# Kernel optimization log

Hardware: AMD Instinct MI355X
Metric: run time of the kernel (lower is better)

The kernel has to match this reference:

```python
import jax, jax.numpy as jnp
import numpy as np

B, L, H, N, CH = 8, 2048, 512, 64, 1


def setup_inputs() -> dict:
    key = jax.random.key(0)
    ks = jax.random.split(key, 7)
    # S4D-Lin style init: w = -0.5 + i*pi*n, with slight noise on the real part
    w_re = -(0.5 + 0.1 * jax.random.uniform(ks[0], (H, N), dtype=jnp.float32))
    w_im = jnp.broadcast_to(jnp.pi * jnp.arange(N, dtype=jnp.float32), (H, N)).copy()
    C_re = jax.random.normal(ks[1], (CH, H, N), dtype=jnp.float32)
    C_im = jax.random.normal(ks[2], (CH, H, N), dtype=jnp.float32)
    D = jax.random.normal(ks[3], (CH, H), dtype=jnp.float32)
    # log-uniform dt in [1e-3, 1e-1]
    log_dt = jax.random.uniform(ks[4], (H,), dtype=jnp.float32,
                                minval=jnp.log(1e-3), maxval=jnp.log(1e-1))
    dt = jnp.exp(log_dt)
    u = jax.random.normal(ks[5], (B, L, H), dtype=jnp.float32)
    return {"u": u, "w_re": w_re, "w_im": w_im, "C_re": C_re,
            "C_im": C_im, "D": D, "dt": dt}


def reference(u, w_re, w_im, C_re, C_im, D, dt):
    # u: [B, L, H] -> [B, H, L]
    uT = jnp.swapaxes(u, -1, -2)
    l = uT.shape[-1]
    h = dt.shape[-1]
    w = (w_re + 1j * w_im).astype(jnp.complex64)          # [t, n]
    v = h // w.shape[0]
    w = jnp.tile(w, (v, 1))                                # [h, n]
    C = (C_re + 1j * C_im).astype(jnp.complex64)           # [c, h, n]
    # --- kernel generation ---
    dtA = w * dt[:, None]                                  # [h, n]
    K = jnp.arange(l) * dtA[..., None]                     # [h, n, l]
    Cs = C * ((jnp.exp(dtA) - 1.0) / w)                    # [c, h, n]
    k = 2.0 * jnp.einsum('chn,hnl->chl', Cs, jnp.exp(K)).real  # [c, h, l]
    # --- FFT convolution ---
    k_f = jnp.fft.rfft(k, n=2 * l - 1)                     # [c, h, l]
    u_f = jnp.fft.rfft(uT, n=2 * l - 1)                    # [B, h, l]
    y_f = jnp.einsum('...hl,chl->...chl', u_f, k_f)        # [B, c, h, l]
    y = jnp.fft.irfft(y_f, n=2 * l)[..., :l]               # [B, c, h, l]
    # skip connection
    y = y + jnp.einsum('...hl,ch->...chl', uT, D)
    # '... c h l -> ... l c h'
    return jnp.moveaxis(y, (-3, -2, -1), (-2, -1, -3))
```

## Files before the change

kernel.cpp:

```cpp
#include <hip/hip_runtime.h>
#include <hip/hip_bf16.h>
#include <math.h>


namespace {
constexpr int cB = 8;
constexpr int cL = 2048;
constexpr int cH = 512;
constexpr int cN = 64;
constexpr int M1 = 4095;
constexpr int M2 = 4096;
constexpr int BH = cB * cH;
constexpr int MA = BH + cH;

constexpr size_t S0   = 2 * ((size_t)cH * cN * 6);
constexpr size_t S_B1 = S0;
constexpr size_t S_A  = S_B1 + (size_t)4096 * 2048;
constexpr size_t S_T2 = S_A  + (size_t)MA * 2048;
constexpr size_t S_U  = S_T2 + (size_t)2048 * 4096;
}

typedef __attribute__((ext_vector_type(8))) short short8;
typedef __attribute__((ext_vector_type(4))) float f32x4;

static __device__ inline short f2bf(float x) {
    __hip_bfloat16 h = __float2bfloat16(x);
    return *reinterpret_cast<short*>(&h);
}
static __device__ inline float bf2f(short s) {
    return __uint_as_float(((unsigned int)(unsigned short)s) << 16);
}
static __device__ __forceinline__ void load_lds16(const short* g, short* l) {
    __builtin_amdgcn_global_load_lds(
        (const __attribute__((address_space(1))) void*)g,
        (__attribute__((address_space(3))) void*)l, 16, 0, 0);
}
#define WAIT_LGKM0() do { asm volatile("s_waitcnt lgkmcnt(0)" ::: "memory"); \
                          __builtin_amdgcn_sched_barrier(0); } while (0)
#define WAIT_LGKM(n) do { asm volatile("s_waitcnt lgkmcnt(" #n ")" ::: "memory"); \
                          __builtin_amdgcn_sched_barrier(0); } while (0)
#define WAIT_VM(n)   do { asm volatile("s_waitcnt vmcnt(" #n ")" ::: "memory"); \
                          __builtin_amdgcn_sched_barrier(0); } while (0)
#define BAR() __builtin_amdgcn_s_barrier()

__global__ __launch_bounds__(256) void k_tabs(short* __restrict__ Wb)
{
    int tid = threadIdx.x;
    if (blockIdx.x < 2048) {
        int j  = blockIdx.x;
        int base = (j < 1024) ? 4 * j : (j == 1024 ? 2 : 4 * (2048 - j) + 2);
        int t0 = tid * 8;
        int p0 = (int)(((long)j * t0) % M1);
        float c, s, cs, ss;
        sincosf((6.283185307179586f / (float)M1) * (float)p0, &s, &c);
        sincosf((6.283185307179586f / (float)M1) * (float)j,  &ss, &cs);
        short8 vc, vs;
#pragma unroll
        for (int i = 0; i < 8; ++i) {
            vc[i] = f2bf(c); vs[i] = f2bf(s);
            float tr = c * cs - s * ss;
            s = c * ss + s * cs;
            c = tr;
        }
        *(short8*)&Wb[S_B1 + (size_t)base       * 2048 + t0] = vc;
        *(short8*)&Wb[S_B1 + (size_t)(base + 1) * 2048 + t0] = vs;
    } else {
        int r   = blockIdx.x - 2048;
        int p   = r >> 10, tau = r & 1023;
        int t   = 2 * tau + p;
        int k0  = tid * 8;
        float stepang = (6.283185307179586f / (float)M2) * (float)t;
        float cs, ss; sincosf(stepang, &ss, &cs);
        short8 v;
        if (k0 < 1024) {
            int ph = (k0 * t) & (M2 - 1);
            float c, s; sincosf((6.283185307179586f / (float)M2) * (float)ph, &s, &c);
#pragma unroll
            for (int i = 0; i < 8; ++i) {
                v[i] = f2bf(c);
                float tr = c * cs - s * ss;
                s = c * ss + s * cs;
                c = tr;
            }
        } else {
            int j0 = k0 - 1024;
            int ph = (j0 * t) & (M2 - 1);
            float c, s; sincosf((6.283185307179586f / (float)M2) * (float)ph, &s, &c);
#pragma unroll
            for (int i = 0; i < 8; ++i) {
                int k = k0 + i;
                v[i] = (k == 1024) ? f2bf((tau & 1) ? -1.f : 1.f) : f2bf(s);
                float tr = c * cs - s * ss;
                s = c * ss + s * cs;
                c = tr;
            }
        }
        *(short8*)&Wb[S_T2 + (size_t)r * 2048 + k0] = v;
    }
}

__global__ __launch_bounds__(256) void k_trans(const float* __restrict__ u,
                                               short* __restrict__ Wb)
{
    __shared__ float tile[64][65];
    int t0 = blockIdx.x * 64;
    int h0 = blockIdx.y * 64;
    int b  = blockIdx.z;
    int cx = threadIdx.x & 63, r0 = threadIdx.x >> 6;
#pragma unroll
    for (int i = 0; i < 16; ++i) {
        int row = r0 + i * 4;
        tile[row][cx] = u[((size_t)b * cL + t0 + row) * cH + h0 + cx];
    }
    __syncthreads();
    short* A = Wb + S_A;
#pragma unroll
    for (int i = 0; i < 16; ++i) {
        int hrow = r0 + i * 4;
        A[(size_t)(b * cH + h0 + hrow) * 2048 + t0 + cx] = f2bf(tile[cx][hrow]);
    }
}

__global__ __launch_bounds__(256) void k_kgen(
    const float* __restrict__ w_re, const float* __restrict__ w_im,
    const float* __restrict__ C_re, const float* __restrict__ C_im,
    const float* __restrict__ dt, short* __restrict__ Wb)
{
    __shared__ float md[cN * 6];
    int h = blockIdx.x, tid = threadIdx.x;
    if (tid < cN) {
        int idx = h * cN + tid;
        double dtv = dt[h];
        double wr = w_re[idx], wi = w_im[idx];
        double ar = wr * dtv, ai = wi * dtv;
        double er = exp(ar);
        double zs, zc; sincos(ai, &zs, &zc);
        double zr = er * zc, zi = er * zs;
        double nr = zr - 1.0, ni = zi;
        double inv = 1.0 / (wr * wr + wi * wi);
        double gr = (nr * wr + ni * wi) * inv;
        double gi = (ni * wr - nr * wi) * inv;
        double cr = C_re[idx], ci = C_im[idx];
        md[tid*6+0] = (float)(cr * gr - ci * gi);
        md[tid*6+1] = (float)(cr * gi + ci * gr);
        md[tid*6+2] = (float)zr; md[tid*6+3] = (float)zi;
        md[tid*6+4] = (float)ar; md[tid*6+5] = (float)ai;
    }
    __syncthreads();
    int t0 = tid * 8;
    float acc[8] = {0.f, 0.f, 0.f, 0.f, 0.f, 0.f, 0.f, 0.f};
    for (int n = 0; n < cN; ++n) {
        float csr = md[n*6+0], csi = md[n*6+1];
        float zr  = md[n*6+2], zi  = md[n*6+3];
        float ar  = md[n*6+4], ai  = md[n*6+5];
        float mag = expf(ar * (float)t0);
        double ph = fmod((double)ai * (double)t0, 6.283185307179586);
        float s, c; sincosf((float)ph, &s, &c);
        float pr = mag * c, pi = mag * s;
#pragma unroll
        for (int i = 0; i < 8; ++i) {
            acc[i] += csr * pr - csi * pi;
            float tr = pr * zr - pi * zi;
            pi = pr * zi + pi * zr;
            pr = tr;
        }
    }
    short8 v;
#pragma unroll
    for (int i = 0; i < 8; ++i) v[i] = f2bf(2.f * acc[i]);
    *reinterpret_cast<short8*>(&Wb[S_A + (size_t)(BH + h) * 2048 + t0]) = v;
}

#define MFMA16(AR, BR, ACC) \
    _Pragma("unroll") for (int kk = 0; kk < 2; ++kk) \
    _Pragma("unroll") for (int ni = 0; ni < 2; ++ni) \
    _Pragma("unroll") for (int mi = 0; mi < 4; ++mi) \
        ACC[mi][ni] = __builtin_amdgcn_mfma_f32_16x16x32_bf16(AR[mi][kk], BR[ni][kk], ACC[mi][ni], 0, 0, 0);

__device__ __forceinline__ void gemm8p_core(
    const short* __restrict__ Ag, int lda,
    const short* __restrict__ Bg, int ldb,
    int m0, int n0, int nt, short* lds, f32x4 (&acc)[4][4][2])
{
    const int tid  = threadIdx.x;
    const int wave = tid >> 6, lane = tid & 63;
    const int wm = wave >> 2, wn = wave & 3;
    const int lm = lane & 15, lk = lane >> 4;
    const int srow8 = lane >> 3;
    const int scol  = (lane & 7) * 8;

    auto stage = [&](const short* G, int ldg, int row0, int half, int kt, int sb) {
        short* l0 = lds + sb + (size_t)((kt & 1) * 2 + half) * 8192;
#pragma unroll
        for (int q = 0; q < 2; ++q) {
            int chunk = wave * 2 + q;
            int r = chunk * 8 + srow8;
            int c = scol ^ ((r & 7) << 3);
            load_lds16(G + (size_t)(row0 + half * 128 + r) * ldg + kt * 64 + c,
                       l0 + chunk * 512);
        }
    };
    auto rdA = [&](int qa, int kt, int mi, int kk) -> short8 {
        int rl = wm * 64 + mi * 16 + lm;
        int c  = (kk * 32 + lk * 8) ^ ((rl & 7) << 3);
        return *(const short8*)(lds + (size_t)((kt & 1) * 2 + qa) * 8192 + rl * 64 + c);
    };
    auto rdB = [&](int qb, int kt, int ni, int kk) -> short8 {
        int rl = wn * 32 + ni * 16 + lm;
        int c  = (kk * 32 + lk * 8) ^ ((rl & 7) << 3);
        return *(const short8*)(lds + 32768 + (size_t)((kt & 1) * 2 + qb) * 8192 + rl * 64 + c);
    };

    stage(Ag, lda, m0, 0, 0, 0);
    stage(Bg, ldb, n0, 0, 0, 32768);
    stage(Bg, ldb, n0, 1, 0, 32768);
    stage(Ag, lda, m0, 1, 0, 0);
    stage(Ag, lda, m0, 0, 1, 0);
    stage(Bg, ldb, n0, 0, 1, 32768);
    stage(Bg, ldb, n0, 1, 1, 32768);
    stage(Ag, lda, m0, 1, 1, 0);
    WAIT_VM(12);
    BAR();

    short8 a0[4][2], a1[4][2], b0[2][2], b1[2][2], b0n[2][2];
#pragma unroll
    for (int mi = 0; mi < 4; ++mi) { a0[mi][0] = rdA(0, 0, mi, 0); a0[mi][1] = rdA(0, 0, mi, 1); }
#pragma unroll
    for (int ni = 0; ni < 2; ++ni) { b0[ni][0] = rdB(0, 0, ni, 0); b0[ni][1] = rdB(0, 0, ni, 1); }
    WAIT_VM(8);
    BAR();

    for (int t = 0; t < nt; ++t) {
        const bool st = (t + 2 < nt);
        const bool rd = (t + 1 < nt);
#pragma unroll
        for (int ni = 0; ni < 2; ++ni) { b1[ni][0] = rdB(1, t, ni, 0); b1[ni][1] = rdB(1, t, ni, 1); }
        BAR();
        WAIT_LGKM(4);
        __builtin_amdgcn_s_setprio(1);
        MFMA16(a0, b0, acc[0]);
        __builtin_amdgcn_s_setprio(0);
        BAR();
#pragma unroll
        for (int mi = 0; mi < 4; ++mi) { a1[mi][0] = rdA(1, t, mi, 0); a1[mi][1] = rdA(1, t, mi, 1); }
        if (st) { stage(Ag, lda, m0, 0, t + 2, 0); stage(Bg, ldb, n0, 0, t + 2, 32768); }
        BAR();
        WAIT_LGKM(8);
        __builtin_amdgcn_s_setprio(1);
        MFMA16(a0, b1, acc[1]);
        __builtin_amdgcn_s_setprio(0);
        BAR();
        if (st) stage(Bg, ldb, n0, 1, t + 2, 32768);
        BAR();
        WAIT_LGKM0();
        __builtin_amdgcn_s_setprio(1);
        MFMA16(a1, b1, acc[3]);
        __builtin_amdgcn_s_setprio(0);
        if (st) { WAIT_VM(10); } else { WAIT_VM(0); }
        BAR();
        if (rd) {
#pragma unroll
            for (int mi = 0; mi < 4; ++mi) { a0[mi][0] = rdA(0, t + 1, mi, 0); a0[mi][1] = rdA(0, t + 1, mi, 1); }
#pragma unroll
            for (int ni = 0; ni < 2; ++ni) { b0n[ni][0] = rdB(0, t + 1, ni, 0); b0n[ni][1] = rdB(0, t + 1, ni, 1); }
        }
        if (st) stage(Ag, lda, m0, 1, t + 2, 0);
        BAR();
        __builtin_amdgcn_s_setprio(1);
        MFMA16(a1, b0, acc[2]);
        __builtin_amdgcn_s_setprio(0);
        if (rd) {
#pragma unroll
            for (int ni = 0; ni < 2; ++ni) { b0[ni][0] = b0n[ni][0]; b0[ni][1] = b0n[ni][1]; }
            WAIT_VM(8);
        } else { WAIT_VM(0); }
        BAR();
    }
}

__global__ __launch_bounds__(512, 2) void k_fwd8(short* __restrict__ Wb)
{
    __shared__ short lds_s[65536];
    int xcd = blockIdx.x & 7, idx = blockIdx.x >> 3;
    const int m0 = (((xcd >> 1) << 2) + (idx >> 3)) * 256;
    const int n0 = (((xcd & 1) << 3) + (idx & 7)) * 256;
    const int tid = threadIdx.x;
    const int wave = tid >> 6, lane = tid & 63;
    const int wm = wave >> 2, wn = wave & 3;
    const int lm = lane & 15, lk = lane >> 4;

    f32x4 acc[4][4][2] = {};
    gemm8p_core(Wb + S_A, 2048, Wb + S_B1, 2048, m0, n0, 32, lds_s, acc);

    short* Uw = Wb + S_U;
    const short* KF = Wb + S_U;
    short (*M)[136] = (short(*)[136])lds_s;
    for (int q = 0; q < 4; ++q) {
        __syncthreads();
#pragma unroll
        for (int mi = 0; mi < 4; ++mi)
#pragma unroll
        for (int ni = 0; ni < 2; ++ni)
#pragma unroll
        for (int r = 0; r < 4; ++r)
            M[wm * 64 + mi * 16 + lk * 4 + r][wn * 32 + ni * 16 + lm] =
                f2bf(acc[q][mi][ni][r]);
        __syncthreads();
        const int pq0 = (n0 >> 2) + (q & 1) * 32;
        int rl = tid >> 2;
        int cp = (tid & 3) * 8;
        int rowg = m0 + (q >> 1) * 128 + rl;
        int h = rowg & (cH - 1);
        int colg = n0 + (q & 1) * 128 + cp * 4;
        short8 kf4[4], m4[4];
#pragma unroll
        for (int w = 0; w < 4; ++w) {
            kf4[w] = *(const short8*)&KF[(size_t)(4096 + h) * 4096 + colg + w * 8];
            m4[w]  = *(const short8*)&M[rl][cp * 4 + w * 8];
        }
        short8 vce, vse, vco, vso;
#pragma unroll
        for (int i = 0; i < 8; ++i) {
            int w = i >> 1, o = (i & 1) * 4;
            float C  = bf2f(m4[w][o]),   S  = bf2f(m4[w][o+1]);
            float C2 = bf2f(m4[w][o+2]), S2 = bf2f(m4[w][o+3]);
            float Ck  = bf2f(kf4[w][o]),   Sk  = bf2f(kf4[w][o+1]);
            float Ck2 = bf2f(kf4[w][o+2]), Sk2 = bf2f(kf4[w][o+3]);
            int pp = pq0 + cp + i;
            float scp = (pp == 0 ? 1.0f : 2.0f) * (1.0f / (float)M2);
            float scq = 2.0f / (float)M2;
            float yrp = scp * (Ck * C - Sk * S);
            float yip = scp * (Ck * S + Sk * C);
            float yrq = scq * (Ck2 * C2 - Sk2 * S2);
            float yiq = scq * (Ck2 * S2 + Sk2 * C2);
            float ce, co, se, so;
            if (pp == 0) { ce = yrp; co = yrp; se = yrq; so = yiq; }
            else { ce = yrp + yrq; co = yrp - yrq; se = yip - yiq; so = yip + yiq; }
            vce[i] = f2bf(ce); vco[i] = f2bf(co);
            vse[i] = f2bf(se); vso[i] = f2bf(so);
        }
        size_t base = (size_t)rowg * 4096;
        int kx = pq0 + cp;
        *(short8*)&Uw[base + kx]        = vce;
        *(short8*)&Uw[base + 1024 + kx] = vse;
        *(short8*)&Uw[base + 2048 + kx] = vco;
        *(short8*)&Uw[base + 3072 + kx] = vso;
    }
}

__global__ __launch_bounds__(256, 2) void k_kfg(short* __restrict__ Wb)
{
    __shared__ __align__(16) short As[64][32];
    __shared__ __align__(16) short Bs[128][32];
    const short* A = Wb + S_A;
    const short* B = Wb + S_B1;
    short* U = Wb + S_U;
    const int tid = threadIdx.x;
    const int m0 = 4096 + blockIdx.y * 64, n0 = blockIdx.x * 128;
    const int wave = tid >> 6, lane = tid & 63;
    const int wr = wave >> 1, wc = wave & 1;
    const int lm = lane & 15, lk = lane >> 4;
    const int srowA = tid >> 2,  scolA = (tid & 3) * 8;
    const int srowB = lane >> 2, scolB = (lane & 3) * 8;

    f32x4 acc[2][4] = {};
    for (int k0 = 0; k0 < 2048; k0 += 32) {
        __syncthreads();
        load_lds16(&A[(size_t)(m0 + srowA) * 2048 + k0 + scolA],
                   &As[0][0] + wave * 512);
#pragma unroll
        for (int q = 0; q < 2; ++q) {
            int chunk = wave * 2 + q;
            load_lds16(&B[(size_t)(n0 + chunk * 16 + srowB) * 2048 + k0 + scolB],
                       &Bs[chunk * 16][0]);
        }
        __syncthreads();
        short8 a[2];
#pragma unroll
        for (int mi = 0; mi < 2; ++mi)
            a[mi] = *(const short8*)&As[wr*32 + mi*16 + lm][lk*8];
#pragma unroll
        for (int ni = 0; ni < 4; ++ni) {
            short8 b = *(const short8*)&Bs[wc*64 + ni*16 + lm][lk*8];
#pragma unroll
            for (int mi = 0; mi < 2; ++mi)
                acc[mi][ni] = __builtin_amdgcn_mfma_f32_16x16x32_bf16(a[mi], b, acc[mi][ni], 0, 0, 0);
        }
    }
#pragma unroll
    for (int mi = 0; mi < 2; ++mi)
#pragma unroll
    for (int ni = 0; ni < 4; ++ni)
#pragma unroll
    for (int r = 0; r < 4; ++r) {
        int row = m0 + wr*32 + mi*16 + lk*4 + r;
        int col = n0 + wc*64 + ni*16 + lm;
        U[(size_t)row * 4096 + col] = f2bf(acc[mi][ni][r]);
    }
}

__global__ __launch_bounds__(512, 1) void k_invB(const float* __restrict__ u,
                                                 const float* __restrict__ Dp,
                                                 short* __restrict__ Wb,
                                                 float* __restrict__ out)
{
    __shared__ short lds_s[57344];
    int xcd = blockIdx.x & 7, idx = blockIdx.x >> 3;
    const int m0 = ((((xcd >> 1) << 2) + (idx >> 3))) * 256;
    const int nj = ((xcd & 1) << 3) + (idx & 7);
    const int p  = nj >> 3;
    const int n0 = (nj & 7) * 128;
    const int tid = threadIdx.x;
    const int wave = tid >> 6, lane = tid & 63;
    const int wm = wave >> 2, wn = wave & 3;
    const int lm = lane & 15, lk = lane >> 4;
    const int srow8 = lane >> 3;
    const int scol  = (lane & 7) * 8;
    constexpr int nt = 32;
    short* lds = lds_s;
    const short* Ag = Wb + S_U + (size_t)p * 2048;
    const short* Bg = Wb + S_T2 + (size_t)p * 1024 * 2048;

    auto stageA = [&](int half, int kt) {
        short* l0 = lds + (size_t)((kt & 1) * 2 + half) * 8192;
#pragma unroll
        for (int q = 0; q < 2; ++q) {
            int chunk = wave * 2 + q;
            int r = chunk * 8 + srow8;
            int c = scol ^ ((r & 7) << 3);
            load_lds16(Ag + (size_t)(m0 + half * 128 + r) * 4096 + kt * 64 + c,
                       l0 + chunk * 512);
        }
    };
    auto stageB = [&](int kt, int slot) {
        short* l0 = lds + 32768 + (size_t)slot * 8192;
#pragma unroll
        for (int q = 0; q < 2; ++q) {
            int chunk = wave * 2 + q;
            int r = chunk * 8 + srow8;
            int c = scol ^ ((r & 7) << 3);
            load_lds16(Bg + (size_t)(n0 + r) * 2048 + kt * 64 + c,
                       l0 + chunk * 512);
        }
    };
    auto rdA = [&](int half, int kt, int mi, int kk) -> short8 {
        int rl = wm * 64 + mi * 16 + lm;
        int c  = (kk * 32 + lk * 8) ^ ((rl & 7) << 3);
        return *(const short8*)(lds + (size_t)((kt & 1) * 2 + half) * 8192 + rl * 64 + c);
    };
    auto rdB = [&](int slot, int ni, int kk) -> short8 {
        int rl = wn * 32 + ni * 16 + lm;
        int c  = (kk * 32 + lk * 8) ^ ((rl & 7) << 3);
        return *(const short8*)(lds + 32768 + (size_t)slot * 8192 + rl * 64 + c);
    };

    f32x4 acc[2][4][2] = {};

    stageA(0, 0);
    stageB(0, 0);
    stageA(1, 0);
    stageA(0, 1);
    stageB(1, 1);
    stageB(2, 2);
    WAIT_VM(8);
    BAR();
    short8 a0[4][2], a1[4][2], b[2][2], bn[2][2];
#pragma unroll
    for (int mi = 0; mi < 4; ++mi) { a0[mi][0] = rdA(0, 0, mi, 0); a0[mi][1] = rdA(0, 0, mi, 1); }
#pragma unroll
    for (int ni = 0; ni < 2; ++ni) { b[ni][0] = rdB(0, ni, 0); b[ni][1] = rdB(0, ni, 1); }
    WAIT_VM(4);
    BAR();

    int bs = 0;
    for (int t = 0; t < nt; ++t) {
        const bool r1 = (t + 1 < nt);
        const bool s2 = (t + 2 < nt);
        const bool s3 = (t + 3 < nt);
        const bool tail = (t >= nt - 3);
        const int bs2 = (bs == 2) ? 0 : bs + 1;
#pragma unroll
        for (int mi = 0; mi < 4; ++mi) { a1[mi][0] = rdA(1, t, mi, 0); a1[mi][1] = rdA(1, t, mi, 1); }
        if (r1) stageA(1, t + 1);
        BAR();
        WAIT_LGKM(8);
        __builtin_amdgcn_s_setprio(1);
        MFMA16(a0, b, acc[0]);
        __builtin_amdgcn_s_setprio(0);
        if (tail) { WAIT_VM(0); } else { WAIT_VM(4); }
        BAR();
        if (r1) {
#pragma unroll
            for (int mi = 0; mi < 4; ++mi) { a0[mi][0] = rdA(0, t + 1, mi, 0); a0[mi][1] = rdA(0, t + 1, mi, 1); }
#pragma unroll
            for (int ni = 0; ni < 2; ++ni) { bn[ni][0] = rdB(bs2, ni, 0); bn[ni][1] = rdB(bs2, ni, 1); }
        }
        if (s2) stageA(0, t + 2);
        if (s3) stageB(t + 3, bs);
        BAR();
        if (r1) { WAIT_LGKM(12); } else { WAIT_LGKM0(); }
        __builtin_amdgcn_s_setprio(1);
        MFMA16(a1, b, acc[1]);
        __builtin_amdgcn_s_setprio(0);
        if (r1) {
#pragma unroll
            for (int ni = 0; ni < 2; ++ni) { b[ni][0] = bn[ni][0]; b[ni][1] = bn[ni][1]; }
        }
        if (tail) { WAIT_VM(0); } else { WAIT_VM(4); }
        BAR();
        bs = bs2;
    }

    const int b_  = m0 >> 9;
    const int h00 = m0 & 511;
    float (*T)[132] = (float(*)[132])lds_s;
#pragma unroll
    for (int q = 0; q < 2; ++q) {
        __syncthreads();
#pragma unroll
        for (int mi = 0; mi < 4; ++mi)
#pragma unroll
        for (int ni = 0; ni < 2; ++ni) {
            int tl = wn * 32 + ni * 16 + lm;
            int hl = wm * 64 + mi * 16 + lk * 4;
            *(float4*)&T[tl][hl] = *(float4*)&acc[q][mi][ni];
        }
        __syncthreads();
        int hg = h00 + q * 128 + (tid & 31) * 4;
        float4 dv = *(const float4*)&Dp[hg];
#pragma unroll
        for (int it = 0; it < 8; ++it) {
            int tl = (tid >> 5) + it * 16;
            int tg = 2 * (n0 + tl) + p;
            size_t gidx = ((size_t)b_ * cL + tg) * cH + hg;
            float4 uv = *(const float4*)&u[gidx];
            float4 yv = *(float4*)&T[tl][(tid & 31) * 4];
            yv.x += dv.x * uv.x;
            yv.y += dv.y * uv.y;
            yv.z += dv.z * uv.z;
            yv.w += dv.w * uv.w;
            *(float4*)&out[gidx] = yv;
        }
    }
}

extern "C" void kernel_launch(void* const* d_in, const int* in_sizes, int n_in,
                              void* d_out, int out_size, void* d_ws, size_t ws_size,
                              hipStream_t stream) {
    const float* u    = (const float*)d_in[0];
    const float* w_re = (const float*)d_in[1];
    const float* w_im = (const float*)d_in[2];
    const float* C_re = (const float*)d_in[3];
    const float* C_im = (const float*)d_in[4];
    const float* Dp   = (const float*)d_in[5];
    const float* dt   = (const float*)d_in[6];
    float* out = (float*)d_out;
    short* Wb  = (short*)d_ws;

    hipLaunchKernelGGL(k_tabs,  dim3(4096), dim3(256), 0, stream, Wb);
    hipLaunchKernelGGL(k_trans, dim3(cL / 64, cH / 64, cB), dim3(256), 0, stream, u, Wb);
    hipLaunchKernelGGL(k_kgen,  dim3(cH), dim3(256), 0, stream,
                       w_re, w_im, C_re, C_im, dt, Wb);
    hipLaunchKernelGGL(k_kfg,   dim3(32, 8), dim3(256), 0, stream, Wb);
    hipLaunchKernelGGL(k_fwd8,  dim3(256), dim3(512), 0, stream, Wb);
    hipLaunchKernelGGL(k_invB,  dim3(256), dim3(512), 0, stream, u, Dp, Wb, out);
}
```

Measured before the change: 190.9 us.

## Simplify GEMM main loops to two-phase schedule with fewer barriers

Both MFMA GEMM loops are restructured from the fine-grained 8-phase (and 4-phase) interleaved schedule with partial lgkmcnt waits into a simpler two-phase schedule. All LDS fragment reads for a step are issued up front, followed by a full lgkmcnt wait, and global-to-LDS staging for step t+2 is issued in one block. This cuts the number of barriers and waitcnts per iteration, meant to reduce sync overhead. The cost is less overlap between LDS reads and MFMA work, and it relies on the changed staging order and vmcnt values still being race-free.

```diff
diff --git a/kernel.cpp b/kernel.cpp
--- a/kernel.cpp
+++ b/kernel.cpp
@@ -36,8 +36,6 @@
         (__attribute__((address_space(3))) void*)l, 16, 0, 0);
 }
 #define WAIT_LGKM0() do { asm volatile("s_waitcnt lgkmcnt(0)" ::: "memory"); \
-                          __builtin_amdgcn_sched_barrier(0); } while (0)
-#define WAIT_LGKM(n) do { asm volatile("s_waitcnt lgkmcnt(" #n ")" ::: "memory"); \
                           __builtin_amdgcn_sched_barrier(0); } while (0)
 #define WAIT_VM(n)   do { asm volatile("s_waitcnt vmcnt(" #n ")" ::: "memory"); \
                           __builtin_amdgcn_sched_barrier(0); } while (0)
@@ -177,7 +175,7 @@
     _Pragma("unroll") for (int mi = 0; mi < 4; ++mi) \
         ACC[mi][ni] = __builtin_amdgcn_mfma_f32_16x16x32_bf16(AR[mi][kk], BR[ni][kk], ACC[mi][ni], 0, 0, 0);
 
-__device__ __forceinline__ void gemm8p_core(
+__device__ __forceinline__ void gemm2p_core(
     const short* __restrict__ Ag, int lda,
     const short* __restrict__ Bg, int ldb,
     int m0, int n0, int nt, short* lds, f32x4 (&acc)[4][4][2])
@@ -219,62 +217,49 @@
     stage(Bg, ldb, n0, 0, 1, 32768);
     stage(Bg, ldb, n0, 1, 1, 32768);
     stage(Ag, lda, m0, 1, 1, 0);
-    WAIT_VM(12);
-    BAR();
-
-    short8 a0[4][2], a1[4][2], b0[2][2], b1[2][2], b0n[2][2];
-#pragma unroll
-    for (int mi = 0; mi < 4; ++mi) { a0[mi][0] = rdA(0, 0, mi, 0); a0[mi][1] = rdA(0, 0, mi, 1); }
-#pragma unroll
-    for (int ni = 0; ni < 2; ++ni) { b0[ni][0] = rdB(0, 0, ni, 0); b0[ni][1] = rdB(0, 0, ni, 1); }
     WAIT_VM(8);
     BAR();
+
+    short8 a0[4][2], a1[4][2], b0[2][2], b1[2][2];
+#pragma unroll
+    for (int mi = 0; mi < 4; ++mi) { a0[mi][0] = rdA(0, 0, mi, 0); a0[mi][1] = rdA(0, 0, mi, 1); }
+#pragma unroll
+    for (int ni = 0; ni < 2; ++ni) { b0[ni][0] = rdB(0, 0, ni, 0); b0[ni][1] = rdB(0, 0, ni, 1); }
 
     for (int t = 0; t < nt; ++t) {
         const bool st = (t + 2 < nt);
         const bool rd = (t + 1 < nt);
 #pragma unroll
         for (int ni = 0; ni < 2; ++ni) { b1[ni][0] = rdB(1, t, ni, 0); b1[ni][1] = rdB(1, t, ni, 1); }
+#pragma unroll
+        for (int mi = 0; mi < 4; ++mi) { a1[mi][0] = rdA(1, t, mi, 0); a1[mi][1] = rdA(1, t, mi, 1); }
         BAR();
-        WAIT_LGKM(4);
+        WAIT_LGKM0();
         __builtin_amdgcn_s_setprio(1);
         MFMA16(a0, b0, acc[0]);
-        __builtin_amdgcn_s_setprio(0);
-        BAR();
-#pragma unroll
-        for (int mi = 0; mi < 4; ++mi) { a1[mi][0] = rdA(1, t, mi, 0); a1[mi][1] = rdA(1, t, mi, 1); }
-        if (st) { stage(Ag, lda, m0, 0, t + 2, 0); stage(Bg, ldb, n0, 0, t + 2, 32768); }
-        BAR();
-        WAIT_LGKM(8);
-        __builtin_amdgcn_s_setprio(1);
         MFMA16(a0, b1, acc[1]);
         __builtin_amdgcn_s_setprio(0);
         BAR();
-        if (st) stage(Bg, ldb, n0, 1, t + 2, 32768);
+        if (st) {
+            stage(Ag, lda, m0, 0, t + 2, 0);
+            stage(Bg, ldb, n0, 0, t + 2, 32768);
+            stage(Bg, ldb, n0, 1, t + 2, 32768);
+            stage(Ag, lda, m0, 1, t + 2, 0);
+            WAIT_VM(8);
+        } else {
+            WAIT_VM(0);
+        }
         BAR();
-        WAIT_LGKM0();
         __builtin_amdgcn_s_setprio(1);
         MFMA16(a1, b1, acc[3]);
-        __builtin_amdgcn_s_setprio(0);
-        if (st) { WAIT_VM(10); } else { WAIT_VM(0); }
-        BAR();
-        if (rd) {
-#pragma unroll
-            for (int mi = 0; mi < 4; ++mi) { a0[mi][0] = rdA(0, t + 1, mi, 0); a0[mi][1] = rdA(0, t + 1, mi, 1); }
-#pragma unroll
-            for (int ni = 0; ni < 2; ++ni) { b0n[ni][0] = rdB(0, t + 1, ni, 0); b0n[ni][1] = rdB(0, t + 1, ni, 1); }
-        }
-        if (st) stage(Ag, lda, m0, 1, t + 2, 0);
-        BAR();
-        __builtin_amdgcn_s_setprio(1);
         MFMA16(a1, b0, acc[2]);
         __builtin_amdgcn_s_setprio(0);
         if (rd) {
 #pragma unroll
-            for (int ni = 0; ni < 2; ++ni) { b0[ni][0] = b0n[ni][0]; b0[ni][1] = b0n[ni][1]; }
-            WAIT_VM(8);
-        } else { WAIT_VM(0); }
-        BAR();
+            for (int mi = 0; mi < 4; ++mi) { a0[mi][0] = rdA(0, t + 1, mi, 0); a0[mi][1] = rdA(0, t + 1, mi, 1); }
+#pragma unroll
+            for (int ni = 0; ni < 2; ++ni) { b0[ni][0] = rdB(0, t + 1, ni, 0); b0[ni][1] = rdB(0, t + 1, ni, 1); }
+        }
     }
 }
 
@@ -290,7 +275,7 @@
     const int lm = lane & 15, lk = lane >> 4;
 
     f32x4 acc[4][4][2] = {};
-    gemm8p_core(Wb + S_A, 2048, Wb + S_B1, 2048, m0, n0, 32, lds_s, acc);
+    gemm2p_core(Wb + S_A, 2048, Wb + S_B1, 2048, m0, n0, 32, lds_s, acc);
 
     short* Uw = Wb + S_U;
     const short* KF = Wb + S_U;
@@ -460,17 +445,16 @@
     stageB(0, 0);
     stageA(1, 0);
     stageA(0, 1);
+    stageA(1, 1);
     stageB(1, 1);
     stageB(2, 2);
     WAIT_VM(8);
     BAR();
-    short8 a0[4][2], a1[4][2], b[2][2], bn[2][2];
+    short8 a0[4][2], a1[4][2], b[2][2];
 #pragma unroll
     for (int mi = 0; mi < 4; ++mi) { a0[mi][0] = rdA(0, 0, mi, 0); a0[mi][1] = rdA(0, 0, mi, 1); }
 #pragma unroll
     for (int ni = 0; ni < 2; ++ni) { b[ni][0] = rdB(0, ni, 0); b[ni][1] = rdB(0, ni, 1); }
-    WAIT_VM(4);
-    BAR();
 
     int bs = 0;
     for (int t = 0; t < nt; ++t) {
@@ -481,33 +465,25 @@
         const int bs2 = (bs == 2) ? 0 : bs + 1;
 #pragma unroll
         for (int mi = 0; mi < 4; ++mi) { a1[mi][0] = rdA(1, t, mi, 0); a1[mi][1] = rdA(1, t, mi, 1); }
-        if (r1) stageA(1, t + 1);
         BAR();
-        WAIT_LGKM(8);
+        WAIT_LGKM0();
         __builtin_amdgcn_s_setprio(1);
         MFMA16(a0, b, acc[0]);
         __builtin_amdgcn_s_setprio(0);
-        if (tail) { WAIT_VM(0); } else { WAIT_VM(4); }
         BAR();
-        if (r1) {
-#pragma unroll
-            for (int mi = 0; mi < 4; ++mi) { a0[mi][0] = rdA(0, t + 1, mi, 0); a0[mi][1] = rdA(0, t + 1, mi, 1); }
-#pragma unroll
-            for (int ni = 0; ni < 2; ++ni) { bn[ni][0] = rdB(bs2, ni, 0); bn[ni][1] = rdB(bs2, ni, 1); }
-        }
-        if (s2) stageA(0, t + 2);
+        if (s2) { stageA(1, t + 2); stageA(0, t + 2); }
         if (s3) stageB(t + 3, bs);
+        if (tail) { WAIT_VM(0); } else { WAIT_VM(6); }
         BAR();
-        if (r1) { WAIT_LGKM(12); } else { WAIT_LGKM0(); }
         __builtin_amdgcn_s_setprio(1);
         MFMA16(a1, b, acc[1]);
         __builtin_amdgcn_s_setprio(0);
         if (r1) {
 #pragma unroll
-            for (int ni = 0; ni < 2; ++ni) { b[ni][0] = bn[ni][0]; b[ni][1] = bn[ni][1]; }
-        }
-        if (tail) { WAIT_VM(0); } else { WAIT_VM(4); }
-        BAR();
+            for (int mi = 0; mi < 4; ++mi) { a0[mi][0] = rdA(0, t + 1, mi, 0); a0[mi][1] = rdA(0, t + 1, mi, 1); }
+#pragma unroll
+            for (int ni = 0; ni < 2; ++ni) { b[ni][0] = rdB(bs2, ni, 0); b[ni][1] = rdB(bs2, ni, 1); }
+        }
         bs = bs2;
     }
 
```

Measured after the change: 190.3 us (median of 2 runs). Within noise of the previous version (-0.3%).
